# Optimization experiments

Hardware: AMD Instinct MI355X
Metric: run time of the kernel (lower is better)

## Reference

```python
import jax, jax.numpy as jnp
import numpy as np

NUM_LAYERS = 3
H = 128          # hidden_dim
COMP_DIM = 128
PROT_DIM = 128
EPS = 1e-6


def setup_inputs() -> dict:
    key = jax.random.key(0)
    ks = jax.random.split(key, 20)
    B, Lc, Lp = 16, 512, 4096
    s = 0.05
    inp = {
        "comp_feat": jax.random.normal(ks[0], (B, Lc, COMP_DIM), jnp.float32),
        "comp_mask": jax.random.randint(ks[1], (B, Lc), 0, 2, jnp.int32),
        "prot_feat": jax.random.normal(ks[2], (B, Lp, PROT_DIM), jnp.float32),
        "prot_mask": jax.random.randint(ks[3], (B, Lp), 0, 2, jnp.int32),
        # per-layer params, stacked on leading layer axis. Linear(x) = x @ W + b
        # (W stored already transposed relative to torch's [out,in] layout).
        "Wc": jax.random.normal(ks[4], (NUM_LAYERS, COMP_DIM, H), jnp.float32) * s,
        "bc": jnp.zeros((NUM_LAYERS, H), jnp.float32),
        "Wp": jax.random.normal(ks[5], (NUM_LAYERS, PROT_DIM, H), jnp.float32) * s,
        "bp": jnp.zeros((NUM_LAYERS, H), jnp.float32),
        "Wbl": jax.random.normal(ks[6], (NUM_LAYERS, H, H), jnp.float32) * s,  # bilinear, no bias
        "Wac": jax.random.normal(ks[7], (NUM_LAYERS, H), jnp.float32) * s,    # Linear(H,1) weight
        "bac": jnp.zeros((NUM_LAYERS,), jnp.float32),
        "Wap": jax.random.normal(ks[8], (NUM_LAYERS, H), jnp.float32) * s,
        "bap": jnp.zeros((NUM_LAYERS,), jnp.float32),
        "Wcomb_c": jax.random.normal(ks[9], (NUM_LAYERS * H, H), jnp.float32) * s,
        "bcomb_c": jnp.zeros((H,), jnp.float32),
        "Wcomb_p": jax.random.normal(ks[10], (NUM_LAYERS * H, H), jnp.float32) * s,
        "bcomb_p": jnp.zeros((H,), jnp.float32),
    }
    return inp


def _masked_softmax(scores, mask):
    # faithful to torch: max over ALL entries (mask applied post-exp), +1e-6 denom
    m = jnp.max(scores, axis=-1, keepdims=True)
    e = jnp.exp(scores - m) * mask
    return e / (jnp.sum(e, axis=-1, keepdims=True) + EPS)


def reference(comp_feat, comp_mask, prot_feat, prot_mask,
              Wc, bc, Wp, bp, Wbl, Wac, bac, Wap, bap,
              Wcomb_c, bcomb_c, Wcomb_p, bcomb_p):
    cm = comp_mask.astype(jnp.float32)  # [B,Lc]
    pm = prot_mask.astype(jnp.float32)  # [B,Lp]
    comp_pooled_list, prot_pooled_list = [], []
    comp_context = prot_context = None
    for i in range(NUM_LAYERS):
        comp_proj = jnp.tanh(comp_feat @ Wc[i] + bc[i])   # [B,Lc,H]
        prot_proj = jnp.tanh(prot_feat @ Wp[i] + bp[i])   # [B,Lp,H]
        comp_bil = comp_proj @ Wbl[i]                      # [B,Lc,H]
        scores = jnp.einsum('bqh,bkh->bqk', comp_bil, prot_proj)  # [B,Lc,Lp]
        scores = scores * (cm[:, :, None] * pm[:, None, :])
        # broadcast-multiply-sum in torch == matmul; same math, efficient form
        comp_context = jnp.einsum('bqk,bkh->bqh', scores, prot_proj)  # [B,Lc,H]
        prot_context = jnp.einsum('bqk,bqh->bkh', scores, comp_proj)  # [B,Lp,H]
        cw = _masked_softmax(comp_context @ Wac[i] + bac[i], cm)  # [B,Lc]
        pw = _masked_softmax(prot_context @ Wap[i] + bap[i], pm)  # [B,Lp]
        comp_pooled_list.append(jnp.einsum('bqh,bq->bh', comp_proj, cw))
        prot_pooled_list.append(jnp.einsum('bkh,bk->bh', prot_proj, pw))
    comp_final = jnp.concatenate(comp_pooled_list, axis=1) @ Wcomb_c + bcomb_c
    prot_final = jnp.concatenate(prot_pooled_list, axis=1) @ Wcomb_p + bcomb_p
    # contexts returned are from the last layer (matches torch loop-variable leak)
    return (comp_final, prot_final, comp_context, prot_context)
```

## Files before the change

kernel.cpp:

```cpp
#include <hip/hip_runtime.h>
#include <math.h>

#define B_ 16
#define LC_ 512
#define LP_ 4096
#define H_ 128
#define HH_ (H_*H_)

typedef unsigned long long u64t;
typedef unsigned short u16t;
typedef __attribute__((ext_vector_type(8))) short bf16x8;
typedef __attribute__((ext_vector_type(4))) float f32x4;

__device__ __forceinline__ u16t f2bf(float f) {
    union { float f; unsigned u; } v; v.f = f;
    unsigned r = (v.u + 0x7FFFu + ((v.u >> 16) & 1u)) >> 16;
    return (u16t)r;
}
__device__ __forceinline__ float bf2f(u16t s) {
    union { unsigned u; float f; } v; v.u = ((unsigned)s) << 16; return v.f;
}
__device__ __forceinline__ float bflo(unsigned u) {
    union { unsigned u; float f; } v; v.u = u << 16; return v.f;
}
__device__ __forceinline__ float bfhi(unsigned u) {
    union { unsigned u; float f; } v; v.u = u & 0xffff0000u; return v.f;
}
__device__ __forceinline__ unsigned cvtpk2(float a, float b) {
    unsigned r;
    asm volatile("v_cvt_pk_bf16_f32 %0, %1, %2" : "=v"(r) : "v"(a), "v"(b));
    return r;
}
__device__ __forceinline__ float ftanh(float x) {
    float e = __expf(2.f * x);
    return fmaf(-2.f, __builtin_amdgcn_rcpf(e + 1.f), 1.f);
}
__device__ __forceinline__ bf16x8 ldfragS(const short* base, int r, int k, int stride) {
    const u64t* p = (const u64t*)(base + (size_t)r * stride + k);
    union { bf16x8 v; u64t q[2]; } u;
    u.q[0] = p[0]; u.q[1] = p[1];
    return u.v;
}
__device__ __forceinline__ bf16x8 ldfragG(const u16t* p) {
    union { bf16x8 v; uint4 q; } u;
    u.q = *(const uint4*)p;
    return u.v;
}

__device__ __forceinline__ void wprep_body(const float* __restrict__ src,
                                           u16t* __restrict__ h, int t) {
    const int n = t >> 1, k0 = (t & 1) * 64;
#pragma unroll 4
    for (int k = 0; k < 64; ++k) {
        float v = src[(size_t)(k0 + k) * H_ + n];
        h[(size_t)n * H_ + k0 + k] = f2bf(v);
    }
}

__global__ __launch_bounds__(256) void prep_k(const float* __restrict__ s0,
                                              const float* __restrict__ s1,
                                              const float* __restrict__ s2,
                                              u16t* __restrict__ hi,
                                              float* __restrict__ zcp,
                                              float* __restrict__ zout) {
    const int bid = blockIdx.x, t = threadIdx.x;
    if (bid < 9) {
        const int grp = bid / 3, lay = bid % 3;
        const float* src = (grp == 0 ? s0 : grp == 1 ? s1 : s2) + (size_t)lay * HH_;
        wprep_body(src, hi + (size_t)bid * HH_, t);
    } else {
        float4 zero = make_float4(0.f, 0.f, 0.f, 0.f);
        float4* z = (float4*)zcp;
        for (int j = t; j < 3072; j += 256) z[j] = zero;
        float4* z2 = (float4*)zout;
        for (int j = t; j < 1024; j += 256) z2[j] = zero;
    }
}

template<int ROWS>
__device__ __forceinline__ void stage_fp32(const float* __restrict__ X,
                                           short* __restrict__ Xs, int t) {
#pragma unroll
    for (int j = 0; j < ROWS / 16; ++j) {
        int lin = j * 512 + t;
        int row = lin >> 5, c4 = lin & 31;
        float4 v = ((const float4*)X)[lin];
        u64t pk = (u64t)cvtpk2(v.x, v.y) | ((u64t)cvtpk2(v.z, v.w) << 32);
        *(u64t*)(Xs + (size_t)row * 136 + c4 * 4) = pk;
    }
}
__device__ __forceinline__ void stage_bf16(const u16t* __restrict__ X,
                                           short* __restrict__ Xs, int t) {
#pragma unroll
    for (int j = 0; j < 4; ++j) {
        int lin = j * 512 + t;
        *(uint4*)(Xs + (lin >> 4) * 136 + (lin & 15) * 8) = ((const uint4*)X)[lin];
    }
}

template<int NRG, bool TANH, bool BF16OUT, bool LDSOUT, bool HILO>
__device__ __forceinline__ void gemm_core(const short* __restrict__ Xs,
                                          const u16t* __restrict__ Whi,
                                          const u16t* __restrict__ Wlo,
                                          const float* __restrict__ bias,
                                          const int* __restrict__ mrow,
                                          void* __restrict__ Yrow0,
                                          short* __restrict__ projLds, int t) {
    const int l = t & 63, w = t >> 6;
    const int lm = l & 15, lk = (l >> 4) * 8, lr = (l >> 4) * 4;
    const int wcol = w * 16;
    const size_t wrow = (size_t)(wcol + lm) * H_;
    bf16x8 wh[4], wl[4];
#pragma unroll
    for (int i = 0; i < 4; ++i) wh[i] = ldfragG(Whi + wrow + i * 32 + lk);
    if (HILO) {
#pragma unroll
        for (int i = 0; i < 4; ++i) wl[i] = ldfragG(Wlo + wrow + i * 32 + lk);
    }
    f32x4 acc[NRG] = {};
#pragma unroll
    for (int i = 0; i < 4; ++i) {
#pragma unroll
        for (int rg = 0; rg < NRG; ++rg) {
            bf16x8 xb = ldfragS(Xs, rg * 16 + lm, i * 32 + lk, 136);
            acc[rg] = __builtin_amdgcn_mfma_f32_16x16x32_bf16(wh[i], xb, acc[rg], 0, 0, 0);
            if (HILO)
                acc[rg] = __builtin_amdgcn_mfma_f32_16x16x32_bf16(wl[i], xb, acc[rg], 0, 0, 0);
        }
    }
    if (LDSOUT) __syncthreads();
    const int col = wcol + lr;
    float4 bq = make_float4(0.f, 0.f, 0.f, 0.f);
    if (bias) bq = *(const float4*)(bias + col);
#pragma unroll
    for (int rg = 0; rg < NRG; ++rg) {
        const int row = rg * 16 + lm;
        float v0 = acc[rg][0] + bq.x, v1 = acc[rg][1] + bq.y;
        float v2 = acc[rg][2] + bq.z, v3 = acc[rg][3] + bq.w;
        if (TANH) { v0 = ftanh(v0); v1 = ftanh(v1); v2 = ftanh(v2); v3 = ftanh(v3); }
        if (mrow) {
            const float msc = (float)mrow[row];
            v0 *= msc; v1 *= msc; v2 *= msc; v3 *= msc;
        }
        if (BF16OUT) {
            u64t pk = (u64t)cvtpk2(v0, v1) | ((u64t)cvtpk2(v2, v3) << 32);
            *(u64t*)((u16t*)Yrow0 + (size_t)row * H_ + col) = pk;
            if (LDSOUT) *(u64t*)(projLds + (size_t)row * 136 + col) = pk;
        } else {
            float4 o; o.x = v0; o.y = v1; o.z = v2; o.w = v3;
            *(float4*)((float*)Yrow0 + (size_t)row * H_ + col) = o;
        }
    }
}

__global__ __launch_bounds__(512) void gemmB_k(const float* __restrict__ prot_feat,
                                               const float* __restrict__ comp_feat,
                                               const u16t* __restrict__ WHi,
                                               const float* __restrict__ bp,
                                               const float* __restrict__ bc,
                                               u16t* __restrict__ prot_proj,
                                               u16t* __restrict__ comp_proj,
                                               u16t* __restrict__ comp_bil) {
    extern __shared__ __align__(16) short smem[];
    const int t = threadIdx.x, bx = blockIdx.x;
    if (bx < 128) {
        short* Xs = smem;
        short* Ys = smem + 64 * 136;
        const long row0 = (long)bx * 64;
        stage_fp32<64>(comp_feat + (size_t)row0 * H_, Xs, t);
        __syncthreads();
#pragma unroll 1
        for (int lay = 0; lay < 3; ++lay) {
            gemm_core<4, true, true, true, false>(Xs, WHi + (size_t)(3 + lay) * HH_,
                nullptr, bc + lay * H_, nullptr,
                comp_proj + ((size_t)lay * B_ * LC_ + row0) * H_, Ys, t);
            __syncthreads();
            gemm_core<4, false, true, false, false>(Ys, WHi + (size_t)(6 + lay) * HH_,
                nullptr, nullptr, nullptr,
                comp_bil + ((size_t)lay * B_ * LC_ + row0) * H_, nullptr, t);
        }
    } else {
        short* Xs = smem;
        const long row0 = (long)(bx - 128) * 128;
        stage_fp32<128>(prot_feat + (size_t)row0 * H_, Xs, t);
        __syncthreads();
#pragma unroll 1
        for (int lay = 0; lay < 3; ++lay)
            gemm_core<8, true, true, false, false>(Xs, WHi + (size_t)lay * HH_,
                nullptr, bp + lay * H_, nullptr,
                prot_proj + ((size_t)lay * B_ * LP_ + row0) * H_, nullptr, t);
    }
}

__device__ __forceinline__ void stage64_bf(const u16t* __restrict__ src,
                                           const int* __restrict__ maskrow,
                                           short* __restrict__ dst, int t) {
    const int m = t & 31, kq = t >> 5;
#pragma unroll
    for (int p = 0; p < 2; ++p) {
        const int kc = p * 32 + kq * 4;
        u64t q[4];
#pragma unroll
        for (int r = 0; r < 4; ++r) {
            u64t v = *(const u64t*)(src + (size_t)(kc + r) * H_ + m * 4);
            if (maskrow && !maskrow[kc + r]) v = 0;
            q[r] = v;
        }
#pragma unroll
        for (int i = 0; i < 4; ++i) {
            u64t val = ((q[0] >> (16 * i)) & 0xffffull)
                     | (((q[1] >> (16 * i)) & 0xffffull) << 16)
                     | (((q[2] >> (16 * i)) & 0xffffull) << 32)
                     | (((q[3] >> (16 * i)) & 0xffffull) << 48);
            *(u64t*)(dst + (size_t)(4 * m + i) * 68 + kc) = val;
        }
    }
}

#define SL_P 4
#define SL_C 2

__global__ __launch_bounds__(256) void syrkC_k(const u16t* __restrict__ prot_proj,
                                               const u16t* __restrict__ comp_bil,
                                               const u16t* __restrict__ comp_proj,
                                               const int* __restrict__ prot_mask,
                                               const int* __restrict__ comp_mask,
                                               float* __restrict__ partP,
                                               float* __restrict__ partC) {
    __shared__ __align__(16) short smem[2 * 128 * 68];
    const int t = threadIdx.x;
    const int slice = blockIdx.x, b = blockIdx.y, z = blockIdx.z;
    const bool isP = z < 3;
    const int slices = isP ? SL_P : SL_C;
    if (slice >= slices) return;
    const int lay = isP ? z : z - 3;
    const u16t* Xl = isP ? prot_proj : comp_bil;
    const u16t* Yr = isP ? prot_proj : comp_proj;
    const int* mask = isP ? prot_mask : comp_mask;
    const int Kb = isP ? LP_ : LC_;
    const int rps = Kb / slices;
    float* part = isP ? partP : partC;
    short* Xt = smem;
    short* Yt = isP ? smem : smem + 128 * 68;

    const int l = t & 63, w = t >> 6;
    const int qi = (w >> 1) * 64, qj = (w & 1) * 64;
    const int lm = l & 15, lk = (l >> 4) * 8, lr = (l >> 4) * 4;
    f32x4 acc[4][4] = {};
    const int chunks = rps >> 6;
    const size_t doff = ((size_t)lay * B_ + b) * Kb;
    const size_t moff = (size_t)b * Kb;

    for (int c = 0; c < chunks; ++c) {
        const int kbase = slice * rps + c * 64;
        stage64_bf(Xl + (doff + kbase) * H_, mask + moff + kbase, Xt, t);
        if (!isP) stage64_bf(Yr + (doff + kbase) * H_, nullptr, Yt, t);
        __syncthreads();
#pragma unroll
        for (int ks = 0; ks < 64; ks += 32) {
            bf16x8 af[4], bfr[4];
#pragma unroll
            for (int it = 0; it < 4; ++it) af[it] = ldfragS(Xt, qi + it * 16 + lm, ks + lk, 68);
#pragma unroll
            for (int jt = 0; jt < 4; ++jt) bfr[jt] = ldfragS(Yt, qj + jt * 16 + lm, ks + lk, 68);
#pragma unroll
            for (int it = 0; it < 4; ++it)
#pragma unroll
                for (int jt = 0; jt < 4; ++jt)
                    acc[it][jt] = __builtin_amdgcn_mfma_f32_16x16x32_bf16(
                        af[it], bfr[jt], acc[it][jt], 0, 0, 0);
        }
        __syncthreads();
    }

    float* pb = part + (((size_t)lay * slices + slice) * B_ + b) * HH_;
#pragma unroll
    for (int it = 0; it < 4; ++it)
#pragma unroll
        for (int jt = 0; jt < 4; ++jt)
#pragma unroll
            for (int r = 0; r < 4; ++r)
                pb[(size_t)(qi + it * 16 + lr + r) * H_ + qj + jt * 16 + lm] = acc[it][jt][r];
}

__global__ __launch_bounds__(256) void reduceC_k(const float4* __restrict__ partP,
                                                 const float4* __restrict__ partC,
                                                 const float* __restrict__ Wac,
                                                 const float* __restrict__ Wap,
                                                 float* __restrict__ vc, float* __restrict__ vp,
                                                 u16t* __restrict__ MNhi, u16t* __restrict__ MNlo) {
    const int lay = blockIdx.y, z = blockIdx.z, t = threadIdx.x;
    const int slices = z ? SL_C : SL_P;
    const size_t quarter = (size_t)B_ * HH_ / 4;
    const float4* p = (z ? partC : partP) + (size_t)lay * slices * quarter;
    const size_t idx = (size_t)blockIdx.x * 256 + t;
    float4 a = p[idx];
    for (int s = 1; s < slices; ++s) {
        float4 v = p[(size_t)s * quarter + idx];
        a.x += v.x; a.y += v.y; a.z += v.z; a.w += v.w;
    }
    const int b = (int)(idx >> 12);
    const int q = (int)(idx & 4095);
    const int row = q >> 5, c4 = q & 31;

    const float* Wv = (z ? Wap : Wac) + lay * H_;
    float4 w4 = ((const float4*)Wv)[c4];
    float s = a.x * w4.x + a.y * w4.y + a.z * w4.z + a.w * w4.w;
#pragma unroll
    for (int o = 16; o > 0; o >>= 1) s += __shfl_down(s, o, 32);
    if ((t & 31) == 0)
        (z ? vp : vc)[((size_t)lay * B_ + b) * H_ + row] = s;

    if (lay == 2) {
        u16t* hi = MNhi + ((size_t)z * B_ + b) * HH_;
        u16t* lo = MNlo + ((size_t)z * B_ + b) * HH_;
        const int colb = c4 * 4;
        float av[4] = {a.x, a.y, a.z, a.w};
#pragma unroll
        for (int j = 0; j < 4; ++j) {
            u16t hh = f2bf(av[j]);
            hi[(size_t)(colb + j) * H_ + row] = hh;
            lo[(size_t)(colb + j) * H_ + row] = f2bf(av[j] - bf2f(hh));
        }
    }
}

__global__ __launch_bounds__(256) void logitsC_k(const u16t* __restrict__ prot_proj,
                                                 const u16t* __restrict__ comp_bil,
                                                 const int* __restrict__ prot_mask,
                                                 const int* __restrict__ comp_mask,
                                                 const float* __restrict__ vp,
                                                 const float* __restrict__ vc,
                                                 const float* __restrict__ bap,
                                                 const float* __restrict__ bac,
                                                 float* __restrict__ logp,
                                                 float* __restrict__ logc) {
    const int zz = blockIdx.z;
    const bool isP = zz < 3;
    if (!isP && blockIdx.x >= LC_ / 256) return;
    const int lay = isP ? zz : zz - 3;
    const int b = blockIdx.y, t = threadIdx.x;
    const int n = isP ? LP_ : LC_;
    __shared__ float v[H_];
    if (t < 128) v[t] = (isP ? vp : vc)[((size_t)lay * B_ + b) * H_ + t];
    __syncthreads();
    const int r = blockIdx.x * 256 + t;
    const u16t* feat = (isP ? prot_proj : comp_bil) + (((size_t)lay * B_ + b) * n + r) * H_;
    const uint2* f2 = (const uint2*)feat;
    const float4* v4 = (const float4*)v;
    float acc = 0.f;
#pragma unroll
    for (int h4 = 0; h4 < 32; ++h4) {
        uint2 u = f2[h4];
        float4 c = v4[h4];
        acc = fmaf(bflo(u.x), c.x, acc); acc = fmaf(bfhi(u.x), c.y, acc);
        acc = fmaf(bflo(u.y), c.z, acc); acc = fmaf(bfhi(u.y), c.w, acc);
    }
    const int mk = (isP ? prot_mask : comp_mask)[(size_t)b * n + r];
    (isP ? logp : logc)[((size_t)lay * B_ + b) * n + r] = (float)mk * acc + (isP ? bap : bac)[lay];
}

__global__ __launch_bounds__(256) void softmaxC_k(const float* __restrict__ logp,
                                                  const float* __restrict__ logc,
                                                  const int* __restrict__ prot_mask,
                                                  const int* __restrict__ comp_mask,
                                                  float* __restrict__ pw,
                                                  float* __restrict__ cw) {
    const int b = blockIdx.x, zz = blockIdx.y, t = threadIdx.x;
    const bool isP = zz < 3;
    const int lay = isP ? zz : zz - 3;
    const int n = isP ? LP_ : LC_;
    const float* l = (isP ? logp : logc) + ((size_t)lay * B_ + b) * n;
    const int* mk = (isP ? prot_mask : comp_mask) + (size_t)b * n;
    float* ww = (isP ? pw : cw) + ((size_t)lay * B_ + b) * n;
    __shared__ float Es[LP_];
    __shared__ float red[4];

    float mx = -1e30f;
    for (int q = t; q < n; q += 256) { float x = l[q]; Es[q] = x; mx = fmaxf(mx, x); }
#pragma unroll
    for (int o = 32; o > 0; o >>= 1) mx = fmaxf(mx, __shfl_down(mx, o, 64));
    if ((t & 63) == 0) red[t >> 6] = mx;
    __syncthreads();
    float m = fmaxf(fmaxf(red[0], red[1]), fmaxf(red[2], red[3]));
    __syncthreads();

    float s = 0.f;
    for (int q = t; q < n; q += 256) {
        float e = __expf(Es[q] - m) * (float)mk[q];
        Es[q] = e;
        s += e;
    }
#pragma unroll
    for (int o = 32; o > 0; o >>= 1) s += __shfl_down(s, o, 64);
    if ((t & 63) == 0) red[t >> 6] = s;
    __syncthreads();
    float denom = red[0] + red[1] + red[2] + red[3] + 1e-6f;
    for (int q = t; q < n; q += 256) ww[q] = Es[q] / denom;
}

__global__ __launch_bounds__(256) void poolC_k(const u16t* __restrict__ prot_proj,
                                               const u16t* __restrict__ comp_proj,
                                               const float* __restrict__ pw,
                                               const float* __restrict__ cw,
                                               float* __restrict__ pp, float* __restrict__ cp) {
    const int zz = blockIdx.z;
    const bool isP = zz < 3;
    if (!isP && blockIdx.y >= 4) return;
    const int lay = isP ? zz : zz - 3;
    const int n = isP ? LP_ : LC_;
    const int chunk = isP ? 256 : 128;
    const int b = blockIdx.x, t = threadIdx.x;
    const int th = t & 63, tq = t >> 6;
    const int q0 = blockIdx.y * chunk;
    const u16t* pb = (isP ? prot_proj : comp_proj) + (((size_t)lay * B_ + b) * n + q0) * H_;
    const float* wb = (isP ? pw : cw) + ((size_t)lay * B_ + b) * n + q0;
    float a0 = 0.f, a1 = 0.f;
    for (int q = tq; q < chunk; q += 4) {
        float wq = wb[q];
        unsigned u = *(const unsigned*)(pb + (size_t)q * H_ + th * 2);
        a0 = fmaf(bflo(u), wq, a0);
        a1 = fmaf(bfhi(u), wq, a1);
    }
    float* ob = (isP ? pp : cp) + ((size_t)lay * B_ + b) * H_;
    atomicAdd(&ob[th * 2], a0);
    atomicAdd(&ob[th * 2 + 1], a1);
}

__global__ __launch_bounds__(512) void ctxC_k(const u16t* __restrict__ comp_bil,
                                              const u16t* __restrict__ prot_proj,
                                              const u16t* __restrict__ MNhi,
                                              const u16t* __restrict__ MNlo,
                                              const int* __restrict__ comp_mask,
                                              const int* __restrict__ prot_mask,
                                              float* __restrict__ out_cc,
                                              float* __restrict__ out_pc) {
    __shared__ __align__(16) short Xs[128 * 136];
    const int t = threadIdx.x, z = blockIdx.z;
    const bool isC = z < 16;
    if (isC && blockIdx.x >= LC_ / 128) return;
    const int b = isC ? z : z - 16;
    const int n = isC ? LC_ : LP_;
    const size_t rowoff = (size_t)b * n + (size_t)blockIdx.x * 128;
    const u16t* X = (isC ? comp_bil + (size_t)2 * B_ * LC_ * H_
                         : prot_proj + (size_t)2 * B_ * LP_ * H_) + rowoff * H_;
    const u16t* Whi = MNhi + ((size_t)(isC ? 0 : 1) * B_ + b) * HH_;
    const u16t* Wlo = MNlo + ((size_t)(isC ? 0 : 1) * B_ + b) * HH_;
    const int* mrow = (isC ? comp_mask : prot_mask) + rowoff;
    float* Y = (isC ? out_cc : out_pc) + rowoff * H_;
    stage_bf16(X, Xs, t);
    __syncthreads();
    gemm_core<8, false, false, false, true>(Xs, Whi, Wlo, nullptr, mrow, Y, nullptr, t);
}

__global__ void finalC_k(const float* __restrict__ cp, const float* __restrict__ pp,
                         const float* __restrict__ Wcc, const float* __restrict__ bcc,
                         const float* __restrict__ Wcp, const float* __restrict__ bcp,
                         float* __restrict__ out_cf, float* __restrict__ out_pf) {
    const int z = blockIdx.z;
    const float* pooled = z ? pp : cp;
    const float* Wcomb = z ? Wcp : Wcc;
    const float* bcomb = z ? bcp : bcc;
    float* out = z ? out_pf : out_cf;
    const int b = blockIdx.x, h = threadIdx.x, j0 = blockIdx.y * 64;
    float acc = (blockIdx.y == 0) ? bcomb[h] : 0.f;
#pragma unroll 4
    for (int j = 0; j < 64; ++j) {
        int jj = j0 + j;
        int lay = jj >> 7, hh = jj & 127;
        acc = fmaf(pooled[((size_t)lay * B_ + b) * H_ + hh], Wcomb[(size_t)jj * H_ + h], acc);
    }
    atomicAdd(&out[b * H_ + h], acc);
}

extern "C" void kernel_launch(void* const* d_in, const int* in_sizes, int n_in,
                              void* d_out, int out_size, void* d_ws, size_t ws_size,
                              hipStream_t stream) {
    const float* comp_feat = (const float*)d_in[0];
    const int*   comp_mask = (const int*)d_in[1];
    const float* prot_feat = (const float*)d_in[2];
    const int*   prot_mask = (const int*)d_in[3];
    const float* Wc      = (const float*)d_in[4];
    const float* bc      = (const float*)d_in[5];
    const float* Wp      = (const float*)d_in[6];
    const float* bp      = (const float*)d_in[7];
    const float* Wbl     = (const float*)d_in[8];
    const float* Wac     = (const float*)d_in[9];
    const float* bac     = (const float*)d_in[10];
    const float* Wap     = (const float*)d_in[11];
    const float* bap     = (const float*)d_in[12];
    const float* Wcomb_c = (const float*)d_in[13];
    const float* bcomb_c = (const float*)d_in[14];
    const float* Wcomb_p = (const float*)d_in[15];
    const float* bcomb_p = (const float*)d_in[16];

    u16t* prot_proj = (u16t*)d_ws;
    u16t* comp_proj = prot_proj + (size_t)3 * B_ * LP_ * H_;
    u16t* comp_bil  = comp_proj + (size_t)3 * B_ * LC_ * H_;
    u16t* WHi  = comp_bil + (size_t)3 * B_ * LC_ * H_;
    u16t* MNhi = WHi + (size_t)9 * HH_;
    u16t* MNlo = MNhi + (size_t)32 * HH_;
    float* f = (float*)(MNlo + (size_t)32 * HH_);
    float* vc = f;    f += (size_t)3 * B_ * H_;
    float* vp = f;    f += (size_t)3 * B_ * H_;
    float* logc = f;  f += (size_t)3 * B_ * LC_;
    float* logp = f;  f += (size_t)3 * B_ * LP_;
    float* cw = f;    f += (size_t)3 * B_ * LC_;
    float* pw = f;    f += (size_t)3 * B_ * LP_;
    float* cp = f;    f += 3 * B_ * H_;
    float* pp = f;    f += 3 * B_ * H_;
    float* partP = pp + 3 * B_ * H_;
    float* partC = partP + (size_t)3 * SL_P * B_ * HH_;

    float* out_cf = (float*)d_out;
    float* out_pf = out_cf + B_ * H_;
    float* out_cc = out_pf + B_ * H_;
    float* out_pc = out_cc + (size_t)B_ * LC_ * H_;

    prep_k<<<dim3(10), 256, 0, stream>>>(Wp, Wc, Wbl, WHi, cp, out_cf);
    gemmB_k<<<dim3(128 + 512), 512, 34816, stream>>>(
        prot_feat, comp_feat, WHi, bp, bc, prot_proj, comp_proj, comp_bil);
    syrkC_k<<<dim3(SL_P, B_, 6), 256, 0, stream>>>(
        prot_proj, comp_bil, comp_proj, prot_mask, comp_mask, partP, partC);
    reduceC_k<<<dim3(256, 3, 2), 256, 0, stream>>>(
        (const float4*)partP, (const float4*)partC, Wac, Wap, vc, vp, MNhi, MNlo);
    logitsC_k<<<dim3(LP_ / 256, B_, 6), 256, 0, stream>>>(
        prot_proj, comp_bil, prot_mask, comp_mask, vp, vc, bap, bac, logp, logc);
    softmaxC_k<<<dim3(B_, 6), 256, 0, stream>>>(logp, logc, prot_mask, comp_mask, pw, cw);
    poolC_k<<<dim3(B_, 16, 6), 256, 0, stream>>>(prot_proj, comp_proj, pw, cw, pp, cp);
    ctxC_k<<<dim3(LP_ / 128, 1, 32), 512, 0, stream>>>(
        comp_bil, prot_proj, MNhi, MNlo, comp_mask, prot_mask, out_cc, out_pc);
    finalC_k<<<dim3(B_, 6, 2), 128, 0, stream>>>(
        cp, pp, Wcomb_c, bcomb_c, Wcomb_p, bcomb_p, out_cf, out_pf);
}
```

Baseline: 179.7 us.

## Prefetch next K-chunk into registers and raise split-K slice counts

Splits the shared-memory staging into a global-load phase and a transpose-write phase, so the next 64-row chunk is loaded into registers while MFMAs run on the current chunk. It also raises the split-K slice counts for the prot and comp SYRK partial products from 4/2 to 16/8, giving more blocks to fill the GPU. The cost is higher register pressure and four times more partial Gram matrices written and later reduced.

```diff
diff --git a/kernel.cpp b/kernel.cpp
--- a/kernel.cpp
+++ b/kernel.cpp
@@ -192,33 +192,40 @@
     }
 }
 
-__device__ __forceinline__ void stage64_bf(const u16t* __restrict__ src,
+__device__ __forceinline__ void stage_load(const u16t* __restrict__ src,
                                            const int* __restrict__ maskrow,
-                                           short* __restrict__ dst, int t) {
+                                           u64t (&q)[2][4], int t) {
     const int m = t & 31, kq = t >> 5;
 #pragma unroll
     for (int p = 0; p < 2; ++p) {
         const int kc = p * 32 + kq * 4;
-        u64t q[4];
 #pragma unroll
         for (int r = 0; r < 4; ++r) {
             u64t v = *(const u64t*)(src + (size_t)(kc + r) * H_ + m * 4);
             if (maskrow && !maskrow[kc + r]) v = 0;
-            q[r] = v;
-        }
+            q[p][r] = v;
+        }
+    }
+}
+__device__ __forceinline__ void stage_write(const u64t (&q)[2][4],
+                                            short* __restrict__ dst, int t) {
+    const int m = t & 31, kq = t >> 5;
+#pragma unroll
+    for (int p = 0; p < 2; ++p) {
+        const int kc = p * 32 + kq * 4;
 #pragma unroll
         for (int i = 0; i < 4; ++i) {
-            u64t val = ((q[0] >> (16 * i)) & 0xffffull)
-                     | (((q[1] >> (16 * i)) & 0xffffull) << 16)
-                     | (((q[2] >> (16 * i)) & 0xffffull) << 32)
-                     | (((q[3] >> (16 * i)) & 0xffffull) << 48);
+            u64t val = ((q[p][0] >> (16 * i)) & 0xffffull)
+                     | (((q[p][1] >> (16 * i)) & 0xffffull) << 16)
+                     | (((q[p][2] >> (16 * i)) & 0xffffull) << 32)
+                     | (((q[p][3] >> (16 * i)) & 0xffffull) << 48);
             *(u64t*)(dst + (size_t)(4 * m + i) * 68 + kc) = val;
         }
     }
 }
 
-#define SL_P 4
-#define SL_C 2
+#define SL_P 16
+#define SL_C 8
 
 __global__ __launch_bounds__(256) void syrkC_k(const u16t* __restrict__ prot_proj,
                                                const u16t* __restrict__ comp_bil,
@@ -251,11 +258,21 @@
     const size_t doff = ((size_t)lay * B_ + b) * Kb;
     const size_t moff = (size_t)b * Kb;
 
+    u64t qx[2][4], qy[2][4];
+    {
+        const int k0 = slice * rps;
+        stage_load(Xl + (doff + k0) * H_, mask + moff + k0, qx, t);
+        if (!isP) stage_load(Yr + (doff + k0) * H_, nullptr, qy, t);
+    }
     for (int c = 0; c < chunks; ++c) {
-        const int kbase = slice * rps + c * 64;
-        stage64_bf(Xl + (doff + kbase) * H_, mask + moff + kbase, Xt, t);
-        if (!isP) stage64_bf(Yr + (doff + kbase) * H_, nullptr, Yt, t);
+        stage_write(qx, Xt, t);
+        if (!isP) stage_write(qy, Yt, t);
         __syncthreads();
+        if (c + 1 < chunks) {
+            const int kn = slice * rps + (c + 1) * 64;
+            stage_load(Xl + (doff + kn) * H_, mask + moff + kn, qx, t);
+            if (!isP) stage_load(Yr + (doff + kn) * H_, nullptr, qy, t);
+        }
 #pragma unroll
         for (int ks = 0; ks < 64; ks += 32) {
             bf16x8 af[4], bfr[4];
```

Result: faster. 174.1 us (-3.1%).
